# Kernel optimization log

Measured on AMD Instinct MI355X. Metric: run time of the kernel, lower is better.

The kernel has to match this reference:

```python
import jax, jax.numpy as jnp
import numpy as np

EPS = 1e-6


def _expand_mask(mask, D, H, W):
    # mask: (B,1,f,f,f) bool -> (B,1,D,H,W) via repeat_interleave on each spatial axis
    m = jnp.repeat(mask, D // mask.shape[2], axis=2)
    m = jnp.repeat(m, H // mask.shape[3], axis=3)
    m = jnp.repeat(m, W // mask.shape[4], axis=4)
    return m


def setup_inputs() -> dict:
    key = jax.random.key(0)
    ks = jax.random.split(key, 10)
    B, C, D, H, W = 2, 192, 32, 32, 32
    K, HID = 7, 4 * C
    x = jax.random.normal(ks[0], (B, C, D, H, W), dtype=jnp.float32)
    mask = jax.random.randint(ks[1], (B, 1, 8, 8, 8), 0, 2) > 0
    dw_w = jax.random.normal(ks[2], (C, 1, K, K, K), dtype=jnp.float32) * (1.0 / np.sqrt(K**3))
    dw_b = jnp.zeros((C,), dtype=jnp.float32)
    ln_w = jnp.ones((C,), dtype=jnp.float32)
    ln_b = jnp.zeros((C,), dtype=jnp.float32)
    w1 = jax.random.normal(ks[3], (C, HID), dtype=jnp.float32) * (1.0 / np.sqrt(C))
    b1 = jnp.zeros((HID,), dtype=jnp.float32)
    w2 = jax.random.normal(ks[4], (HID, C), dtype=jnp.float32) * (1.0 / np.sqrt(HID))
    b2 = jnp.zeros((C,), dtype=jnp.float32)
    gamma = jnp.full((C,), 1e-6, dtype=jnp.float32)
    return {"x": x, "mask": mask, "dw_w": dw_w, "dw_b": dw_b, "ln_w": ln_w,
            "ln_b": ln_b, "w1": w1, "b1": b1, "w2": w2, "b2": b2, "gamma": gamma}


def reference(x, mask, dw_w, dw_b, ln_w, ln_b, w1, b1, w2, b2, gamma):
    B, C, D, H, W = x.shape
    m = _expand_mask(mask, D, H, W)              # (B,1,D,H,W) bool
    mf = m.astype(x.dtype)

    # depthwise 3D conv, SAME padding (padding = kernel//2), groups = C
    y = jax.lax.conv_general_dilated(
        x, dw_w, window_strides=(1, 1, 1), padding='SAME',
        dimension_numbers=('NCDHW', 'OIDHW', 'NCDHW'),
        feature_group_count=C)
    y = y + dw_b[None, :, None, None, None]

    # channels_last: (B,D,H,W,C)
    y = jnp.transpose(y, (0, 2, 3, 4, 1))

    # sparse LayerNorm over channel dim: normalize all tokens, keep only active
    # (equivalent to gather->LN->scatter-into-zeros in the original)
    mu = jnp.mean(y, axis=-1, keepdims=True)
    var = jnp.mean(jnp.square(y - mu), axis=-1, keepdims=True)
    ln = (y - mu) * jax.lax.rsqrt(var + EPS) * ln_w + ln_b
    ln = ln * jnp.transpose(mf, (0, 2, 3, 4, 1))  # zero inactive tokens

    # pointwise MLP
    h = jax.nn.gelu(jnp.einsum('bdhwc,ce->bdhwe', ln, w1) + b1, approximate=False)
    o = jnp.einsum('bdhwe,ec->bdhwc', h, w2) + b2
    o = gamma * o

    # back to channels_first and final sparse mask
    o = jnp.transpose(o, (0, 4, 1, 2, 3)) * mf
    return o
```

## Files before the change

### kernel.cpp

```cpp
#include <hip/hip_runtime.h>
#include <hip/hip_bf16.h>

typedef __attribute__((ext_vector_type(2))) float f2v;
typedef __attribute__((ext_vector_type(4))) float f4v;
typedef __attribute__((ext_vector_type(8))) short bf8v;

#define NPOS 32768
#define CCH  192
#define HID  768

#define WS_Y    ((size_t)0)
#define WS_B1F  ((size_t)25165824)
#define WS_B2F  ((size_t)25460736)
#define WS_WP2  ((size_t)25755648)
#define WS_TOTAL ((size_t)26357760)

__device__ inline unsigned short f2bf(float f){
  unsigned int u = __float_as_uint(f);
  u += 0x7FFFu + ((u >> 16) & 1u);
  return (unsigned short)(u >> 16);
}
__device__ inline float bf2f(unsigned short s){
  return __uint_as_float(((unsigned int)s) << 16);
}
__device__ inline float gelu_f(float x){
  float u = 0.7978845608028654f * x * fmaf(0.044715f, x*x, 1.0f);
  float e = __expf(2.0f*u);
  float th = __fdividef(e - 1.0f, e + 1.0f);
  return 0.5f*x*(1.0f + th);
}

#define PKFMA_L(A, X, W) \
  asm("v_pk_fma_f32 %0, %2, %1, %0 op_sel:[0,0,0] op_sel_hi:[1,0,1]" \
      : "+v"(A) : "v"(X), "s"(W))
#define PKFMA_H(A, X, W) \
  asm("v_pk_fma_f32 %0, %2, %1, %0 op_sel:[0,1,0] op_sel_hi:[1,1,1]" \
      : "+v"(A) : "v"(X), "s"(W))

template<int ASMP>
__global__ __launch_bounds__(256) void conv_dw_kernel(
    const float* __restrict__ x, const float* __restrict__ dw_w,
    const float* __restrict__ dw_b, const double* __restrict__ wpair2,
    unsigned short* __restrict__ yc)
{
  __shared__ float ring[22*528];

  int bid = blockIdx.x;
  int c = bid % 192;
  int r = bid / 192;
  int xq = r & 1, yq = (r >> 1) & 1, zh = (r >> 2) & 1, b = r >> 3;
  int tx0 = xq*16, ty0 = yq*16, zb = zh*16;

  int tid = threadIdx.x;
  const float* xsrc = x + ((size_t)(b*CCH + c))*NPOS;

  for (int idx = tid; idx < 2904; idx += 256) {
    int sl = idx / 132;
    int rem = idx - sl*132;
    int rr = rem / 6, ci = rem - rr*6;
    int zi = zb - 3 + sl, gy = ty0 - 3 + rr, gx = tx0 - 4 + 4*ci;
    f4v v = {0.f, 0.f, 0.f, 0.f};
    if ((unsigned)zi < 32u && (unsigned)gy < 32u && (unsigned)gx <= 28u)
      v = *(const f4v*)(xsrc + (size_t)zi*1024 + gy*32 + gx);
    *(f4v*)(ring + sl*528 + rr*24 + ci*4) = v;
  }
  __syncthreads();

  int p = tid & 15, zl = tid >> 4;
  int px = p & 3, py = p >> 2;
  int y0 = py*4, px4 = px*4;
  const float* base = ring + zl*528 + y0*24 + px4;

  if constexpr (ASMP) {
    const double* wb2 = wpair2 + (size_t)c*392;

    double acc[8];
    #pragma unroll
    for (int i = 0; i < 8; ++i) acc[i] = 0.0;

    #pragma unroll 1
    for (int s = 0; s < 7; ++s) {
      const float* sb = base + s*528;
      const double* wrow = wb2 + s*56;
      #pragma unroll
      for (int rr = 0; rr < 10; ++rr) {
        const float* rb = sb + rr*24;
        union { f4v v; double d[2]; } q0, q1, q2;
        q0.v = *(const f4v*)(rb);
        q1.v = *(const f4v*)(rb + 4);
        q2.v = *(const f4v*)(rb + 8);
        double P[6] = {q0.d[0], q0.d[1], q1.d[0], q1.d[1], q2.d[0], q2.d[1]};
        #pragma unroll
        for (int j = 1; j <= 10; ++j) {
          #pragma unroll
          for (int dy = 0; dy < 4; ++dy) {
            int ky = rr - dy;
            if (ky < 0 || ky > 6) continue;
            if (j <= 8) {
              double w = wrow[ky*8 + (j-1)];
              if (j & 1) { PKFMA_H(acc[dy*2+0], P[j>>1], w); }
              else       { PKFMA_L(acc[dy*2+0], P[j>>1], w); }
            }
            if (j >= 3) {
              double w = wrow[ky*8 + (j-3)];
              if (j & 1) { PKFMA_H(acc[dy*2+1], P[j>>1], w); }
              else       { PKFMA_L(acc[dy*2+1], P[j>>1], w); }
            }
          }
        }
      }
    }

    float bias = dw_b[c];
    int z = zb + zl;
    int cz = z >> 2, cx = (tx0 >> 2) + px, cy = (ty0 >> 2) + py;
    int cell = cz*64 + cy*8 + cx;
    unsigned short* ybase = yc + (((size_t)(b*512 + cell))*192 + c)*64;
    int tokz = (z & 3)*16;
    #pragma unroll
    for (int dy = 0; dy < 4; ++dy) {
      union { double d; float f[2]; } u0, u1;
      u0.d = acc[dy*2+0]; u1.d = acc[dy*2+1];
      ushort4 o;
      o.x = f2bf(u0.f[0] + bias);
      o.y = f2bf(u0.f[1] + bias);
      o.z = f2bf(u1.f[0] + bias);
      o.w = f2bf(u1.f[1] + bias);
      *(ushort4*)(ybase + tokz + dy*4) = o;
    }
  } else {
    const float* wbase = dw_w + (size_t)c*343;
    f2v acc[8];
    #pragma unroll
    for (int i = 0; i < 8; ++i) acc[i] = (f2v){0.f, 0.f};

    #pragma unroll 1
    for (int s = 0; s < 7; ++s) {
      const float* sb = base + s*528;
      f4v n0 = *(const f4v*)(sb);
      f4v n1 = *(const f4v*)(sb + 4);
      f4v n2 = *(const f4v*)(sb + 8);
      #pragma unroll
      for (int rr = 0; rr < 10; ++rr) {
        f4v r0 = n0, r1 = n1, r2 = n2;
        if (rr < 9) {
          n0 = *(const f4v*)(sb + (rr+1)*24);
          n1 = *(const f4v*)(sb + (rr+1)*24 + 4);
          n2 = *(const f4v*)(sb + (rr+1)*24 + 8);
        }
        f2v pr[10];
        pr[1] = (f2v){r0[1], r0[2]};
        pr[2] = (f2v){r0[2], r0[3]};
        pr[3] = (f2v){r0[3], r1[0]};
        pr[4] = (f2v){r1[0], r1[1]};
        pr[5] = (f2v){r1[1], r1[2]};
        pr[6] = (f2v){r1[2], r1[3]};
        pr[7] = (f2v){r1[3], r2[0]};
        pr[8] = (f2v){r2[0], r2[1]};
        pr[9] = (f2v){r2[1], r2[2]};
        #pragma unroll
        for (int dy = 0; dy < 4; ++dy) {
          int ky = rr - dy;
          if (ky < 0 || ky > 6) continue;
          #pragma unroll
          for (int kx = 0; kx < 7; ++kx) {
            float w = wbase[s*49 + ky*7 + kx];
            f2v wv = (f2v){w, w};
            acc[dy*2+0] = __builtin_elementwise_fma(wv, pr[kx+1], acc[dy*2+0]);
            acc[dy*2+1] = __builtin_elementwise_fma(wv, pr[kx+3], acc[dy*2+1]);
          }
        }
      }
    }

    float bias = dw_b[c];
    int z = zb + zl;
    int cz = z >> 2, cx = (tx0 >> 2) + px, cy = (ty0 >> 2) + py;
    int cell = cz*64 + cy*8 + cx;
    unsigned short* ybase = yc + (((size_t)(b*512 + cell))*192 + c)*64;
    int tokz = (z & 3)*16;
    #pragma unroll
    for (int dy = 0; dy < 4; ++dy) {
      ushort4 o;
      o.x = f2bf(acc[dy*2+0][0] + bias);
      o.y = f2bf(acc[dy*2+0][1] + bias);
      o.z = f2bf(acc[dy*2+1][0] + bias);
      o.w = f2bf(acc[dy*2+1][1] + bias);
      *(ushort4*)(ybase + tokz + dy*4) = o;
    }
  }
}

__global__ __launch_bounds__(256) void prep_w_kernel(
    const float* __restrict__ w1, const float* __restrict__ w2,
    const float* __restrict__ dw_w,
    unsigned short* __restrict__ b1f, unsigned short* __restrict__ b2f,
    f2v* __restrict__ wp2)
{
  int gid = blockIdx.x*256 + threadIdx.x;
  if (gid < 18432) {
    int fi = gid;
    int lane = fi & 63, fr = fi >> 6;
    int nt = fr / 6, ks = fr - nt*6;
    int n  = nt*16 + (lane & 15);
    int kb = ks*32 + (lane >> 4)*8;
    #pragma unroll
    for (int j = 0; j < 8; ++j) b1f[fi*8 + j] = f2bf(w1[(kb+j)*HID + n]);
  } else if (gid < 36864) {
    int fi = gid - 18432;
    int lane = fi & 63, fr = fi >> 6;
    int nt = fr / 24, ks = fr - nt*24;
    int n  = nt*16 + (lane & 15);
    int kb = ks*32 + (lane >> 4)*8;
    #pragma unroll
    for (int j = 0; j < 8; ++j) b2f[fi*8 + j] = f2bf(w2[(kb+j)*CCH + n]);
  } else if (gid < 46272) {
    int ci = gid - 36864;
    int cch = ci / 49, t = ci - cch*49;
    const float* wr = dw_w + cch*343 + t*7;
    #pragma unroll
    for (int j = 0; j < 8; ++j) {
      float lo = (j <= 6) ? wr[j] : 0.f;
      float hi = (j >= 1) ? wr[j-1] : 0.f;
      wp2[ci*8 + j] = (f2v){lo, hi};
    }
  }
}

__global__ __launch_bounds__(256) void mlp_kernel(
    const unsigned short* __restrict__ yc, const unsigned short* __restrict__ b1f,
    const unsigned short* __restrict__ b2f, const float* __restrict__ b1,
    const float* __restrict__ b2, const float* __restrict__ gamma,
    const float* __restrict__ ln_w, const float* __restrict__ ln_b,
    const int* __restrict__ mask, float* __restrict__ out)
{
  int bid = blockIdx.x;
  int b = bid >> 9, cell = bid & 511;
  int cz = cell >> 6, cy = (cell >> 3) & 7, cx = cell & 7;
  int z0 = cz*4, y0 = cy*4, x0 = cx*4;
  int tid = threadIdx.x, wave = tid >> 6, lane = tid & 63;
  int lq = lane >> 4, ln15 = lane & 15;

  if (mask[bid] == 0) {
    f4v z4 = {0.f, 0.f, 0.f, 0.f};
    #pragma unroll
    for (int pp = 0; pp < 12; ++pp) {
      int i4 = tid + 256*pp;
      int c = i4 >> 4, rem = i4 & 15;
      int dz = rem >> 2, dy = rem & 3;
      *(f4v*)(out + ((size_t)(b*CCH + c))*NPOS
                  + (size_t)(z0+dz)*1024 + (y0+dy)*32 + x0) = z4;
    }
    return;
  }

  __shared__ __align__(16) char uni[26112];
  unsigned short* ymat = (unsigned short*)uni;
  unsigned short* hbuf = (unsigned short*)uni;
  __shared__ unsigned short aFrag[12288];
  __shared__ float sred[2][4][64];
  __shared__ float murs[2][64];

  const unsigned short* ysrc = yc + (size_t)bid*12288;

  #pragma unroll
  for (int k = 0; k < 12; ++k) {
    int idx = tid + 256*k;
    int c = idx >> 4, t4 = idx & 15;
    *(ushort4*)(ymat + c*68 + t4*4) = *(const ushort4*)(ysrc + c*64 + t4*4);
  }
  __syncthreads();

  {
    int tok = tid & 63, part = tid >> 6;
    float S = 0.f, Q = 0.f;
    #pragma unroll
    for (int j = 0; j < 48; ++j) {
      float v = bf2f(ymat[(part*48 + j)*68 + tok]);
      S += v; Q = fmaf(v, v, Q);
    }
    sred[0][part][tok] = S; sred[1][part][tok] = Q;
  }
  __syncthreads();
  if (tid < 64) {
    float S = sred[0][0][tid] + sred[0][1][tid] + sred[0][2][tid] + sred[0][3][tid];
    float Q = sred[1][0][tid] + sred[1][1][tid] + sred[1][2][tid] + sred[1][3][tid];
    float m = S*(1.f/192.f);
    float var = Q*(1.f/192.f) - m*m;
    murs[0][tid] = m;
    murs[1][tid] = rsqrtf(var + 1e-6f);
  }
  __syncthreads();

  #pragma unroll
  for (int k = 0; k < 6; ++k) {
    int fi = tid + 256*k;
    int lane2 = fi & 63, rest = fi >> 6;
    int mt = rest / 6, ks = rest - mt*6;
    int tok = mt*16 + (lane2 & 15);
    int cc0 = ks*32 + (lane2 >> 4)*8;
    float m = murs[0][tok], rs = murs[1][tok];
    f4v lw0 = *(const f4v*)(ln_w + cc0), lw1 = *(const f4v*)(ln_w + cc0 + 4);
    f4v lb0 = *(const f4v*)(ln_b + cc0), lb1 = *(const f4v*)(ln_b + cc0 + 4);
    union { bf8v v; unsigned short u[8]; } pk;
    #pragma unroll
    for (int j = 0; j < 4; ++j) {
      float v0 = (bf2f(ymat[(cc0+j)*68 + tok])   - m)*rs*lw0[j] + lb0[j];
      float v1 = (bf2f(ymat[(cc0+4+j)*68 + tok]) - m)*rs*lw1[j] + lb1[j];
      pk.u[j] = f2bf(v0); pk.u[4+j] = f2bf(v1);
    }
    *(bf8v*)(aFrag + fi*8) = pk.v;
  }
  __syncthreads();

  f4v acc2[4][3];
  #pragma unroll
  for (int mt = 0; mt < 4; ++mt)
    #pragma unroll
    for (int nt = 0; nt < 3; ++nt)
      acc2[mt][nt] = (f4v){0.f, 0.f, 0.f, 0.f};

  const unsigned short* p1base = b1f + wave*2*3072 + lane*8;
  const unsigned short* p2base = b2f + wave*3*12288 + lane*8;

  bf8v B1r[12];
  #pragma unroll
  for (int i = 0; i < 12; ++i) {
    int jj = i / 6, ks = i - jj*6;
    B1r[i] = *(const bf8v*)(p1base + jj*3072 + ks*512);
  }

  #pragma unroll 1
  for (int ch = 0; ch < 6; ++ch) {
    bf8v B2r[12];
    const unsigned short* p2 = p2base + ch*2048;
    #pragma unroll
    for (int ks2 = 0; ks2 < 4; ++ks2)
      #pragma unroll
      for (int nt = 0; nt < 3; ++nt)
        B2r[ks2*3 + nt] = *(const bf8v*)(p2 + nt*12288 + ks2*512);

    f4v a1[2][4];
    #pragma unroll
    for (int jj = 0; jj < 2; ++jj)
      #pragma unroll
      for (int mt = 0; mt < 4; ++mt) a1[jj][mt] = (f4v){0.f,0.f,0.f,0.f};
    #pragma unroll
    for (int ks = 0; ks < 6; ++ks) {
      bf8v Af[4];
      #pragma unroll
      for (int mt = 0; mt < 4; ++mt)
        Af[mt] = *(const bf8v*)(aFrag + ((mt*6 + ks)*64 + lane)*8);
      #pragma unroll
      for (int jj = 0; jj < 2; ++jj)
        #pragma unroll
        for (int mt = 0; mt < 4; ++mt)
          a1[jj][mt] = __builtin_amdgcn_mfma_f32_16x16x32_bf16(Af[mt], B1r[jj*6+ks], a1[jj][mt], 0, 0, 0);
    }

    if (ch < 5) {
      const unsigned short* p1 = p1base + (ch+1)*24576;
      #pragma unroll
      for (int i = 0; i < 12; ++i) {
        int jj = i / 6, ks = i - jj*6;
        B1r[i] = *(const bf8v*)(p1 + jj*3072 + ks*512);
      }
    }

    #pragma unroll
    for (int jj = 0; jj < 2; ++jj) {
      float b1v = b1[(ch*8 + wave*2 + jj)*16 + ln15];
      int lane_hi = jj*2 + (ln15 >> 3);
      #pragma unroll
      for (int mt = 0; mt < 4; ++mt)
        #pragma unroll
        for (int rr = 0; rr < 4; ++rr) {
          float g = gelu_f(a1[jj][mt][rr] + b1v);
          int elem = ((mt*4 + wave)*64 + lane_hi*16 + (lq*4 + rr))*8 + (lane & 7);
          hbuf[elem] = f2bf(g);
        }
    }
    __syncthreads();
    #pragma unroll
    for (int ks2 = 0; ks2 < 4; ++ks2) {
      bf8v A2[4];
      #pragma unroll
      for (int mt = 0; mt < 4; ++mt)
        A2[mt] = *(const bf8v*)(hbuf + ((mt*4 + ks2)*64 + lane)*8);
      #pragma unroll
      for (int nt = 0; nt < 3; ++nt)
        #pragma unroll
        for (int mt = 0; mt < 4; ++mt)
          acc2[mt][nt] = __builtin_amdgcn_mfma_f32_16x16x32_bf16(A2[mt], B2r[ks2*3+nt], acc2[mt][nt], 0, 0, 0);
    }
    __syncthreads();
  }

  #pragma unroll
  for (int nt = 0; nt < 3; ++nt) {
    int c = (wave*3 + nt)*16 + ln15;
    float gm = gamma[c], bb = b2[c];
    size_t cbase = ((size_t)(b*CCH + c))*NPOS + (size_t)(y0 + lq)*32 + x0;
    #pragma unroll
    for (int mt = 0; mt < 4; ++mt) {
      f4v o;
      o[0] = gm*(acc2[mt][nt][0] + bb);
      o[1] = gm*(acc2[mt][nt][1] + bb);
      o[2] = gm*(acc2[mt][nt][2] + bb);
      o[3] = gm*(acc2[mt][nt][3] + bb);
      *(f4v*)(out + cbase + (size_t)(z0 + mt)*1024) = o;
    }
  }
}

extern "C" void kernel_launch(void* const* d_in, const int* in_sizes, int n_in,
                              void* d_out, int out_size, void* d_ws, size_t ws_size,
                              hipStream_t stream) {
  const float* x     = (const float*)d_in[0];
  const int*   mask  = (const int*)  d_in[1];
  const float* dw_w  = (const float*)d_in[2];
  const float* dw_b  = (const float*)d_in[3];
  const float* ln_w  = (const float*)d_in[4];
  const float* ln_b  = (const float*)d_in[5];
  const float* w1    = (const float*)d_in[6];
  const float* b1    = (const float*)d_in[7];
  const float* w2    = (const float*)d_in[8];
  const float* b2    = (const float*)d_in[9];
  const float* gamma = (const float*)d_in[10];
  float* out = (float*)d_out;
  char* ws = (char*)d_ws;

  unsigned short* yc  = (unsigned short*)(ws + WS_Y);
  unsigned short* b1f = (unsigned short*)(ws + WS_B1F);
  unsigned short* b2f = (unsigned short*)(ws + WS_B2F);
  double*         wp2 = (double*)(ws + WS_WP2);

  bool wp_ok = ws_size >= WS_TOTAL;
  int prep_grid = wp_ok ? 181 : 144;
  prep_w_kernel<<<prep_grid, 256, 0, stream>>>(w1, w2, dw_w, b1f, b2f, (f2v*)wp2);
  if (wp_ok)
    conv_dw_kernel<1><<<3072, 256, 0, stream>>>(x, dw_w, dw_b, wp2, yc);
  else
    conv_dw_kernel<0><<<3072, 256, 0, stream>>>(x, dw_w, dw_b, wp2, yc);
  mlp_kernel<<<1024, 256, 0, stream>>>(yc, b1f, b2f, b1, b2, gamma, ln_w, ln_b, mask, out);
}
```

Before: 282.3 us.

## Run depthwise conv with fp16 dot2 instructions and half-precision LDS tile

Converts the input tile to fp16 when staging it into shared memory and computes the 7x7x7 depthwise conv with v_dot2_f32_f16, accumulating in fp32. Weights are pre-packed as fp16 pairs, with a shifted copy so that each dot2 covers two taps for two output positions. This roughly halves the FMA instruction count and the LDS footprint and traffic compared with the packed fp32 path, and sets a launch-bounds occupancy hint. The cost is fp16 rounding of inputs and weights, which reduces accuracy before the bf16 output.

Measured after the change: 270.3 us. -4.3%, faster.

```diff
diff --git a/kernel.cpp b/kernel.cpp
--- a/kernel.cpp
+++ b/kernel.cpp
@@ -12,7 +12,7 @@
 #define WS_Y    ((size_t)0)
 #define WS_B1F  ((size_t)25165824)
 #define WS_B2F  ((size_t)25460736)
-#define WS_WP2  ((size_t)25755648)
+#define WS_WPF  ((size_t)25755648)
 #define WS_TOTAL ((size_t)26357760)
 
 __device__ inline unsigned short f2bf(float f){
@@ -30,18 +30,99 @@
   return 0.5f*x*(1.0f + th);
 }
 
-#define PKFMA_L(A, X, W) \
-  asm("v_pk_fma_f32 %0, %2, %1, %0 op_sel:[0,0,0] op_sel_hi:[1,0,1]" \
-      : "+v"(A) : "v"(X), "s"(W))
-#define PKFMA_H(A, X, W) \
-  asm("v_pk_fma_f32 %0, %2, %1, %0 op_sel:[0,1,0] op_sel_hi:[1,1,1]" \
-      : "+v"(A) : "v"(X), "s"(W))
-
-template<int ASMP>
-__global__ __launch_bounds__(256) void conv_dw_kernel(
+#define DOT2(A, X, W) \
+  asm("v_dot2_f32_f16 %0, %1, %2, %0" : "+v"(A) : "v"(X), "s"(W))
+
+__global__ __launch_bounds__(256, 6) void conv_dw_f16_kernel(
+    const float* __restrict__ x, const float* __restrict__ dw_b,
+    const unsigned int* __restrict__ wpf, unsigned short* __restrict__ yc)
+{
+  __shared__ unsigned short ring[22*528];
+
+  int bid = blockIdx.x;
+  int c = bid % 192;
+  int r = bid / 192;
+  int xq = r & 1, yq = (r >> 1) & 1, zh = (r >> 2) & 1, b = r >> 3;
+  int tx0 = xq*16, ty0 = yq*16, zb = zh*16;
+
+  int tid = threadIdx.x;
+  const float* xsrc = x + ((size_t)(b*CCH + c))*NPOS;
+
+  for (int idx = tid; idx < 2904; idx += 256) {
+    int sl = idx / 132;
+    int rem = idx - sl*132;
+    int rr = rem / 6, ci = rem - rr*6;
+    int zi = zb - 3 + sl, gy = ty0 - 3 + rr, gx = tx0 - 4 + 4*ci;
+    f4v v = {0.f, 0.f, 0.f, 0.f};
+    if ((unsigned)zi < 32u && (unsigned)gy < 32u && (unsigned)gx <= 28u)
+      v = *(const f4v*)(xsrc + (size_t)zi*1024 + gy*32 + gx);
+    union { _Float16 h[4]; uint2 u2; } pk;
+    pk.h[0] = (_Float16)v[0]; pk.h[1] = (_Float16)v[1];
+    pk.h[2] = (_Float16)v[2]; pk.h[3] = (_Float16)v[3];
+    *(uint2*)(ring + sl*528 + rr*24 + ci*4) = pk.u2;
+  }
+  __syncthreads();
+
+  int p = tid & 15, zl = tid >> 4;
+  int px = p & 3, py = p >> 2;
+  int y0 = py*4, px4 = px*4;
+  const unsigned short* base = ring + zl*528 + y0*24 + px4;
+
+  const unsigned int* wb = wpf + (size_t)c*392;
+
+  float acc[4][4];
+  #pragma unroll
+  for (int i = 0; i < 4; ++i)
+    #pragma unroll
+    for (int j = 0; j < 4; ++j) acc[i][j] = 0.f;
+
+  #pragma unroll 1
+  for (int s = 0; s < 7; ++s) {
+    const unsigned short* sb = base + s*528;
+    const unsigned int* wrow = wb + s*56;
+    #pragma unroll
+    for (int rr = 0; rr < 10; ++rr) {
+      const unsigned short* rb = sb + rr*24;
+      uint2 q0 = *(const uint2*)(rb);
+      uint2 q1 = *(const uint2*)(rb + 4);
+      uint2 q2 = *(const uint2*)(rb + 8);
+      unsigned int D[6] = {q0.x, q0.y, q1.x, q1.y, q2.x, q2.y};
+      #pragma unroll
+      for (int dy = 0; dy < 4; ++dy) {
+        int ky = rr - dy;
+        if (ky < 0 || ky > 6) continue;
+        const unsigned int* wk = wrow + ky*8;
+        #pragma unroll
+        for (int t = 0; t < 4; ++t) {
+          DOT2(acc[dy][0], D[t],   wk[t]);
+          DOT2(acc[dy][1], D[t+1], wk[4+t]);
+          DOT2(acc[dy][2], D[t+1], wk[t]);
+          DOT2(acc[dy][3], D[t+2], wk[4+t]);
+        }
+      }
+    }
+  }
+
+  float bias = dw_b[c];
+  int z = zb + zl;
+  int cz = z >> 2, cx = (tx0 >> 2) + px, cy = (ty0 >> 2) + py;
+  int cell = cz*64 + cy*8 + cx;
+  unsigned short* ybase = yc + (((size_t)(b*512 + cell))*192 + c)*64;
+  int tokz = (z & 3)*16;
+  #pragma unroll
+  for (int dy = 0; dy < 4; ++dy) {
+    ushort4 o;
+    o.x = f2bf(acc[dy][0] + bias);
+    o.y = f2bf(acc[dy][1] + bias);
+    o.z = f2bf(acc[dy][2] + bias);
+    o.w = f2bf(acc[dy][3] + bias);
+    *(ushort4*)(ybase + tokz + dy*4) = o;
+  }
+}
+
+__global__ __launch_bounds__(256) void conv_dw_f32_kernel(
     const float* __restrict__ x, const float* __restrict__ dw_w,
-    const float* __restrict__ dw_b, const double* __restrict__ wpair2,
-    unsigned short* __restrict__ yc)
+    const float* __restrict__ dw_b, unsigned short* __restrict__ yc)
 {
   __shared__ float ring[22*528];
 
@@ -70,124 +151,65 @@
   int px = p & 3, py = p >> 2;
   int y0 = py*4, px4 = px*4;
   const float* base = ring + zl*528 + y0*24 + px4;
-
-  if constexpr (ASMP) {
-    const double* wb2 = wpair2 + (size_t)c*392;
-
-    double acc[8];
-    #pragma unroll
-    for (int i = 0; i < 8; ++i) acc[i] = 0.0;
-
-    #pragma unroll 1
-    for (int s = 0; s < 7; ++s) {
-      const float* sb = base + s*528;
-      const double* wrow = wb2 + s*56;
-      #pragma unroll
-      for (int rr = 0; rr < 10; ++rr) {
-        const float* rb = sb + rr*24;
-        union { f4v v; double d[2]; } q0, q1, q2;
-        q0.v = *(const f4v*)(rb);
-        q1.v = *(const f4v*)(rb + 4);
-        q2.v = *(const f4v*)(rb + 8);
-        double P[6] = {q0.d[0], q0.d[1], q1.d[0], q1.d[1], q2.d[0], q2.d[1]};
+  const float* wbase = dw_w + (size_t)c*343;
+
+  f2v acc[8];
+  #pragma unroll
+  for (int i = 0; i < 8; ++i) acc[i] = (f2v){0.f, 0.f};
+
+  #pragma unroll 1
+  for (int s = 0; s < 7; ++s) {
+    const float* sb = base + s*528;
+    f4v n0 = *(const f4v*)(sb);
+    f4v n1 = *(const f4v*)(sb + 4);
+    f4v n2 = *(const f4v*)(sb + 8);
+    #pragma unroll
+    for (int rr = 0; rr < 10; ++rr) {
+      f4v r0 = n0, r1 = n1, r2 = n2;
+      if (rr < 9) {
+        n0 = *(const f4v*)(sb + (rr+1)*24);
+        n1 = *(const f4v*)(sb + (rr+1)*24 + 4);
+        n2 = *(const f4v*)(sb + (rr+1)*24 + 8);
+      }
+      f2v pr[10];
+      pr[1] = (f2v){r0[1], r0[2]};
+      pr[2] = (f2v){r0[2], r0[3]};
+      pr[3] = (f2v){r0[3], r1[0]};
+      pr[4] = (f2v){r1[0], r1[1]};
+      pr[5] = (f2v){r1[1], r1[2]};
+      pr[6] = (f2v){r1[2], r1[3]};
+      pr[7] = (f2v){r1[3], r2[0]};
+      pr[8] = (f2v){r2[0], r2[1]};
+      pr[9] = (f2v){r2[1], r2[2]};
+      #pragma unroll
+      for (int dy = 0; dy < 4; ++dy) {
+        int ky = rr - dy;
+        if (ky < 0 || ky > 6) continue;
         #pragma unroll
-        for (int j = 1; j <= 10; ++j) {
-          #pragma unroll
-          for (int dy = 0; dy < 4; ++dy) {
-            int ky = rr - dy;
-            if (ky < 0 || ky > 6) continue;
-            if (j <= 8) {
-              double w = wrow[ky*8 + (j-1)];
-              if (j & 1) { PKFMA_H(acc[dy*2+0], P[j>>1], w); }
-              else       { PKFMA_L(acc[dy*2+0], P[j>>1], w); }
-            }
-            if (j >= 3) {
-              double w = wrow[ky*8 + (j-3)];
-              if (j & 1) { PKFMA_H(acc[dy*2+1], P[j>>1], w); }
-              else       { PKFMA_L(acc[dy*2+1], P[j>>1], w); }
-            }
-          }
+        for (int kx = 0; kx < 7; ++kx) {
+          float w = wbase[s*49 + ky*7 + kx];
+          f2v wv = (f2v){w, w};
+          acc[dy*2+0] = __builtin_elementwise_fma(wv, pr[kx+1], acc[dy*2+0]);
+          acc[dy*2+1] = __builtin_elementwise_fma(wv, pr[kx+3], acc[dy*2+1]);
         }
       }
     }
-
-    float bias = dw_b[c];
-    int z = zb + zl;
-    int cz = z >> 2, cx = (tx0 >> 2) + px, cy = (ty0 >> 2) + py;
-    int cell = cz*64 + cy*8 + cx;
-    unsigned short* ybase = yc + (((size_t)(b*512 + cell))*192 + c)*64;
-    int tokz = (z & 3)*16;
-    #pragma unroll
-    for (int dy = 0; dy < 4; ++dy) {
-      union { double d; float f[2]; } u0, u1;
-      u0.d = acc[dy*2+0]; u1.d = acc[dy*2+1];
-      ushort4 o;
-      o.x = f2bf(u0.f[0] + bias);
-      o.y = f2bf(u0.f[1] + bias);
-      o.z = f2bf(u1.f[0] + bias);
-      o.w = f2bf(u1.f[1] + bias);
-      *(ushort4*)(ybase + tokz + dy*4) = o;
-    }
-  } else {
-    const float* wbase = dw_w + (size_t)c*343;
-    f2v acc[8];
-    #pragma unroll
-    for (int i = 0; i < 8; ++i) acc[i] = (f2v){0.f, 0.f};
-
-    #pragma unroll 1
-    for (int s = 0; s < 7; ++s) {
-      const float* sb = base + s*528;
-      f4v n0 = *(const f4v*)(sb);
-      f4v n1 = *(const f4v*)(sb + 4);
-      f4v n2 = *(const f4v*)(sb + 8);
-      #pragma unroll
-      for (int rr = 0; rr < 10; ++rr) {
-        f4v r0 = n0, r1 = n1, r2 = n2;
-        if (rr < 9) {
-          n0 = *(const f4v*)(sb + (rr+1)*24);
-          n1 = *(const f4v*)(sb + (rr+1)*24 + 4);
-          n2 = *(const f4v*)(sb + (rr+1)*24 + 8);
-        }
-        f2v pr[10];
-        pr[1] = (f2v){r0[1], r0[2]};
-        pr[2] = (f2v){r0[2], r0[3]};
-        pr[3] = (f2v){r0[3], r1[0]};
-        pr[4] = (f2v){r1[0], r1[1]};
-        pr[5] = (f2v){r1[1], r1[2]};
-        pr[6] = (f2v){r1[2], r1[3]};
-        pr[7] = (f2v){r1[3], r2[0]};
-        pr[8] = (f2v){r2[0], r2[1]};
-        pr[9] = (f2v){r2[1], r2[2]};
-        #pragma unroll
-        for (int dy = 0; dy < 4; ++dy) {
-          int ky = rr - dy;
-          if (ky < 0 || ky > 6) continue;
-          #pragma unroll
-          for (int kx = 0; kx < 7; ++kx) {
-            float w = wbase[s*49 + ky*7 + kx];
-            f2v wv = (f2v){w, w};
-            acc[dy*2+0] = __builtin_elementwise_fma(wv, pr[kx+1], acc[dy*2+0]);
-            acc[dy*2+1] = __builtin_elementwise_fma(wv, pr[kx+3], acc[dy*2+1]);
-          }
-        }
-      }
-    }
-
-    float bias = dw_b[c];
-    int z = zb + zl;
-    int cz = z >> 2, cx = (tx0 >> 2) + px, cy = (ty0 >> 2) + py;
-    int cell = cz*64 + cy*8 + cx;
-    unsigned short* ybase = yc + (((size_t)(b*512 + cell))*192 + c)*64;
-    int tokz = (z & 3)*16;
-    #pragma unroll
-    for (int dy = 0; dy < 4; ++dy) {
-      ushort4 o;
-      o.x = f2bf(acc[dy*2+0][0] + bias);
-      o.y = f2bf(acc[dy*2+0][1] + bias);
-      o.z = f2bf(acc[dy*2+1][0] + bias);
-      o.w = f2bf(acc[dy*2+1][1] + bias);
-      *(ushort4*)(ybase + tokz + dy*4) = o;
-    }
+  }
+
+  float bias = dw_b[c];
+  int z = zb + zl;
+  int cz = z >> 2, cx = (tx0 >> 2) + px, cy = (ty0 >> 2) + py;
+  int cell = cz*64 + cy*8 + cx;
+  unsigned short* ybase = yc + (((size_t)(b*512 + cell))*192 + c)*64;
+  int tokz = (z & 3)*16;
+  #pragma unroll
+  for (int dy = 0; dy < 4; ++dy) {
+    ushort4 o;
+    o.x = f2bf(acc[dy*2+0][0] + bias);
+    o.y = f2bf(acc[dy*2+0][1] + bias);
+    o.z = f2bf(acc[dy*2+1][0] + bias);
+    o.w = f2bf(acc[dy*2+1][1] + bias);
+    *(ushort4*)(ybase + tokz + dy*4) = o;
   }
 }
 
@@ -195,7 +217,7 @@
     const float* __restrict__ w1, const float* __restrict__ w2,
     const float* __restrict__ dw_w,
     unsigned short* __restrict__ b1f, unsigned short* __restrict__ b2f,
-    f2v* __restrict__ wp2)
+    unsigned int* __restrict__ wpf)
 {
   int gid = blockIdx.x*256 + threadIdx.x;
   if (gid < 18432) {
@@ -216,13 +238,24 @@
     for (int j = 0; j < 8; ++j) b2f[fi*8 + j] = f2bf(w2[(kb+j)*CCH + n]);
   } else if (gid < 46272) {
     int ci = gid - 36864;
-    int cch = ci / 49, t = ci - cch*49;
-    const float* wr = dw_w + cch*343 + t*7;
-    #pragma unroll
-    for (int j = 0; j < 8; ++j) {
-      float lo = (j <= 6) ? wr[j] : 0.f;
-      float hi = (j >= 1) ? wr[j-1] : 0.f;
-      wp2[ci*8 + j] = (f2v){lo, hi};
+    int cch = ci / 49, t7 = ci - cch*49;
+    const float* wr = dw_w + cch*343 + t7*7;
+    float w[8];
+    #pragma unroll
+    for (int j = 0; j < 7; ++j) w[j] = wr[j];
+    w[7] = 0.f;
+    union { _Float16 h[2]; unsigned int u; } pk;
+    #pragma unroll
+    for (int t = 0; t < 4; ++t) {
+      pk.h[0] = (t == 0) ? (_Float16)0.f : (_Float16)w[2*t-1];
+      pk.h[1] = (_Float16)w[2*t];
+      wpf[ci*8 + t] = pk.u;
+    }
+    #pragma unroll
+    for (int t = 0; t < 4; ++t) {
+      pk.h[0] = (_Float16)w[2*t];
+      pk.h[1] = (_Float16)w[2*t+1];
+      wpf[ci*8 + 4 + t] = pk.u;
     }
   }
 }
@@ -433,14 +466,14 @@
   unsigned short* yc  = (unsigned short*)(ws + WS_Y);
   unsigned short* b1f = (unsigned short*)(ws + WS_B1F);
   unsigned short* b2f = (unsigned short*)(ws + WS_B2F);
-  double*         wp2 = (double*)(ws + WS_WP2);
+  unsigned int*   wpf = (unsigned int*)(ws + WS_WPF);
 
   bool wp_ok = ws_size >= WS_TOTAL;
   int prep_grid = wp_ok ? 181 : 144;
-  prep_w_kernel<<<prep_grid, 256, 0, stream>>>(w1, w2, dw_w, b1f, b2f, (f2v*)wp2);
+  prep_w_kernel<<<prep_grid, 256, 0, stream>>>(w1, w2, dw_w, b1f, b2f, wpf);
   if (wp_ok)
-    conv_dw_kernel<1><<<3072, 256, 0, stream>>>(x, dw_w, dw_b, wp2, yc);
+    conv_dw_f16_kernel<<<3072, 256, 0, stream>>>(x, dw_b, wpf, yc);
   else
-    conv_dw_kernel<0><<<3072, 256, 0, stream>>>(x, dw_w, dw_b, wp2, yc);
+    conv_dw_f32_kernel<<<3072, 256, 0, stream>>>(x, dw_w, dw_b, yc);
   mlp_kernel<<<1024, 256, 0, stream>>>(yc, b1f, b2f, b1, b2, gamma, ln_w, ln_b, mask, out);
 }
```
